# Kernel tuning notes

Measured on AMD Instinct MI355X. Metric: run time of the kernel, lower is better.

Reference implementation:

```python
import jax, jax.numpy as jnp
import numpy as np

C, CH, H = 128, 32, 4  # c_in, c_hidden, n_head


def _layer_norm(x, w, b, eps=1e-5):
    mu = jnp.mean(x, axis=-1, keepdims=True)
    var = jnp.var(x, axis=-1, keepdims=True)
    return (x - mu) * jax.lax.rsqrt(var + eps) * w + b


def _tri_attn(x, ln_w, ln_b, wq, wk, wv, wz, wg, bg, wo, bo):
    # x: [B, I, J, C]; attention runs over J independently for each row I
    B, I, J, _ = x.shape
    x = _layer_norm(x, ln_w, ln_b)
    q = (x @ wq).reshape(B, I, J, H, CH) * (CH ** -0.5)
    k = (x @ wk).reshape(B, I, J, H, CH)
    v = (x @ wv).reshape(B, I, J, H, CH)
    # learned pairwise triangle bias: [B, I, J, H] -> [B, 1, H, I, J]
    tb = jnp.transpose(x @ wz, (0, 3, 1, 2))[:, None]
    scores = jnp.einsum('biqhd,bikhd->bihqk', q, k) + tb  # [B, I, H, J, J]
    a = jax.nn.softmax(scores, axis=-1)
    o = jnp.einsum('bihqk,bikhd->biqhd', a, v)
    g = jax.nn.sigmoid(x @ wg + bg).reshape(B, I, J, H, CH)
    o = (o * g).reshape(B, I, J, H * CH)
    return o @ wo + bo


def setup_inputs() -> dict:
    key = jax.random.key(0)
    ks = jax.random.split(key, 16)
    B, N = 1, 256
    inp = {'cmap': jax.random.normal(ks[0], (B, C, N, N), jnp.float32)}
    for i, p in enumerate(['s', 'e']):
        kq, kk, kv, kz, kg, ko = jax.random.split(ks[1 + i], 6)
        sd = 0.02
        inp[p + '_ln_w'] = jnp.ones((C,), jnp.float32)
        inp[p + '_ln_b'] = jnp.zeros((C,), jnp.float32)
        inp[p + '_wq'] = jax.random.normal(kq, (C, H * CH), jnp.float32) * sd
        inp[p + '_wk'] = jax.random.normal(kk, (C, H * CH), jnp.float32) * sd
        inp[p + '_wv'] = jax.random.normal(kv, (C, H * CH), jnp.float32) * sd
        inp[p + '_wz'] = jax.random.normal(kz, (C, H), jnp.float32) * sd
        inp[p + '_wg'] = jax.random.normal(kg, (C, H * CH), jnp.float32) * sd
        inp[p + '_bg'] = jnp.ones((H * CH,), jnp.float32)  # gating bias init = 1
        inp[p + '_wo'] = jax.random.normal(ko, (H * CH, C), jnp.float32) * sd
        inp[p + '_bo'] = jnp.zeros((C,), jnp.float32)
    return inp


def reference(cmap,
              s_ln_w, s_ln_b, s_wq, s_wk, s_wv, s_wz, s_wg, s_bg, s_wo, s_bo,
              e_ln_w, e_ln_b, e_wq, e_wk, e_wv, e_wz, e_wg, e_bg, e_wo, e_bo):
    # cmap: [B, C, I, J] -> channels last [B, I, J, C]
    x = jnp.transpose(cmap, (0, 2, 3, 1))
    # triangle attention around starting node (dropout is identity in eval)
    x = x + _tri_attn(x, s_ln_w, s_ln_b, s_wq, s_wk, s_wv, s_wz, s_wg, s_bg, s_wo, s_bo)
    # triangle attention around ending node: transpose I<->J, attend, transpose back
    xt = jnp.swapaxes(x, 1, 2)
    x = x + jnp.swapaxes(
        _tri_attn(xt, e_ln_w, e_ln_b, e_wq, e_wk, e_wv, e_wz, e_wg, e_bg, e_wo, e_bo), 1, 2)
    return jnp.transpose(x, (0, 3, 1, 2))
```

## Files before the change

### kernel.cpp

```cpp
#include <hip/hip_runtime.h>
#include <hip/hip_bf16.h>

#define NNX 256
#define CCX 128
#define HHX 4
#define CHDX 32
#define NIJ (NNX*NNX)

typedef __hip_bfloat16 bf16;
typedef __hip_bfloat162 bf162;
typedef __attribute__((ext_vector_type(8))) short short8v;
typedef __attribute__((ext_vector_type(4))) float float4v;
typedef __attribute__((ext_vector_type(4))) unsigned int uint4v;

__device__ __forceinline__ float4v MFMA(short8v a, short8v b, float4v c){
  return __builtin_amdgcn_mfma_f32_16x16x32_bf16(a, b, c, 0, 0, 0);
}

__device__ __forceinline__ unsigned pk2(float a, float b){
  unsigned short ua = __bfloat16_as_ushort(__float2bfloat16(a));
  unsigned short ub = __bfloat16_as_ushort(__float2bfloat16(b));
  return (unsigned)ua | ((unsigned)ub << 16);
}
__device__ __forceinline__ float ubf(unsigned short u){
  return __bfloat162float(__ushort_as_bfloat16(u));
}

__global__ __launch_bounds__(256) void k_tout(const float* __restrict__ x, float* __restrict__ out){
  __shared__ float t[32][33];
  const int i = blockIdx.z, jt = blockIdx.x, ct = blockIdx.y;
  const int tx = threadIdx.x, ty = threadIdx.y;
  #pragma unroll
  for(int k=0;k<32;k+=8){
    t[ty+k][tx] = x[((size_t)i*NNX + jt*32+ty+k)*CCX + ct*32 + tx];
  }
  __syncthreads();
  #pragma unroll
  for(int k=0;k<32;k+=8){
    out[(size_t)(ct*32+ty+k)*NIJ + (size_t)i*NNX + jt*32 + tx] = t[tx][ty+k];
  }
}

__global__ __launch_bounds__(256) void k_lntin(const float* __restrict__ cmap,
    const float* __restrict__ w, const float* __restrict__ b,
    const float* __restrict__ wz, float* __restrict__ x,
    bf16* __restrict__ xln, float* __restrict__ tb2){
  __shared__ float t[32][130];
  const int jt = blockIdx.x, i = blockIdx.y;
  const int tx = threadIdx.x, ty = threadIdx.y;
  #pragma unroll
  for(int kk=0; kk<16; ++kk){
    const int c = kk*8 + ty;
    t[tx][c] = cmap[(size_t)c*NIJ + (size_t)i*NNX + jt*32 + tx];
  }
  __syncthreads();
  const int tid = ty*32 + tx;
  const int row = tid >> 3, cs = tid & 7;
  const int c0 = cs*16;
  float v[16];
  #pragma unroll
  for(int u=0;u<16;++u) v[u] = t[row][c0+u];
  float s=0.f, s2=0.f;
  #pragma unroll
  for(int u=0;u<16;++u){ s += v[u]; s2 += v[u]*v[u]; }
  #pragma unroll
  for(int off=4; off>0; off>>=1){ s += __shfl_xor(s,off); s2 += __shfl_xor(s2,off); }
  const float mu = s*0.0078125f;
  const float var = s2*0.0078125f - mu*mu;
  const float rs = rsqrtf(var+1e-5f);
  const int r = i*NNX + jt*32 + row;
  float a[16];
  #pragma unroll
  for(int u=0;u<16;++u) a[u] = (v[u]-mu)*rs*w[c0+u]+b[c0+u];
  float* xd = x + (size_t)r*CCX + c0;
  #pragma unroll
  for(int u4=0;u4<4;++u4){
    float4 f4; f4.x=v[u4*4]; f4.y=v[u4*4+1]; f4.z=v[u4*4+2]; f4.w=v[u4*4+3];
    *(float4*)(xd + u4*4) = f4;
  }
  bf16* xl = xln + (size_t)r*CCX + c0;
  #pragma unroll
  for(int u8=0;u8<4;++u8){
    uint2 pw; pw.x = pk2(a[u8*4], a[u8*4+1]); pw.y = pk2(a[u8*4+2], a[u8*4+3]);
    *(uint2*)(xl + u8*4) = pw;
  }
  float acc[4] = {0.f,0.f,0.f,0.f};
  #pragma unroll
  for(int u=0;u<16;++u){
    #pragma unroll
    for(int hh=0;hh<4;++hh) acc[hh] += a[u]*wz[(c0+u)*4+hh];
  }
  #pragma unroll
  for(int off=4; off>0; off>>=1){
    #pragma unroll
    for(int hh=0;hh<4;++hh) acc[hh] += __shfl_xor(acc[hh], off);
  }
  if(cs==0){
    #pragma unroll
    for(int hh=0;hh<4;++hh) tb2[(size_t)hh*NIJ + r] = acc[hh];
  }
}

template<int TRANS>
__global__ __launch_bounds__(256) void k_lntb(const float* __restrict__ x,
    const float* __restrict__ w, const float* __restrict__ b,
    const float* __restrict__ wz, bf16* __restrict__ xln, float* __restrict__ tb2){
  const int r = blockIdx.x*4 + threadIdx.y;
  const int ii = r>>8, jj = r&255;
  const float* src = x + (size_t)(TRANS ? (jj*NNX+ii) : r)*CCX;
  const int c = threadIdx.x*2;
  float2 v = *(const float2*)(src+c);
  float s = v.x+v.y, s2 = v.x*v.x+v.y*v.y;
  #pragma unroll
  for(int off=32; off>0; off>>=1){ s += __shfl_xor(s,off); s2 += __shfl_xor(s2,off); }
  float mu = s*0.0078125f;
  float var = s2*0.0078125f - mu*mu;
  float rs = rsqrtf(var+1e-5f);
  float a0 = (v.x-mu)*rs*w[c]+b[c];
  float a1 = (v.y-mu)*rs*w[c+1]+b[c+1];
  bf162 hp; hp.x = __float2bfloat16(a0); hp.y = __float2bfloat16(a1);
  *(bf162*)(xln + (size_t)r*CCX + c) = hp;
  float acc[4];
  #pragma unroll
  for(int hh=0;hh<4;++hh) acc[hh] = a0*wz[c*4+hh] + a1*wz[(c+1)*4+hh];
  #pragma unroll
  for(int off=32; off>0; off>>=1){
    #pragma unroll
    for(int hh=0;hh<4;++hh) acc[hh] += __shfl_xor(acc[hh], off);
  }
  if(threadIdx.x==0){
    #pragma unroll
    for(int hh=0;hh<4;++hh) tb2[(size_t)hh*NIJ + r] = acc[hh];
  }
}

__global__ __launch_bounds__(256) void k_cvtw(const float* __restrict__ wq,
    const float* __restrict__ wk, const float* __restrict__ wv,
    const float* __restrict__ wg, const float* __restrict__ wo, bf16* __restrict__ wT){
  int idx = blockIdx.x*256 + threadIdx.x;
  if(idx < 65536){
    int n = idx >> 7, k = idx & 127;
    const float* W = (n<128)?wq:(n<256)?wk:(n<384)?wv:wg;
    wT[idx] = __float2bfloat16(W[k*CCX + (n&127)]);
  } else {
    int idx2 = idx - 65536;
    int n = idx2 >> 7, k = idx2 & 127;
    wT[idx] = __float2bfloat16(wo[k*CCX + n]);
  }
}

template<int SUB>
__device__ __forceinline__ void attn_sub(const int mb,
    const int lq, const int g, const int l,
    uint2 pgl, uint2 pgh,
    const char* qsb, char* ksb, const char* vtb,
    const float* tbq_base, bf16* __restrict__ obh){
  const int q0 = mb + SUB*16;
  const int q  = q0 + lq;
  short8v qf = *(const short8v*)(qsb + (size_t)q*80 + g*16);
  const float* tbq = tbq_base + (size_t)q*NNX;
  float4v s[16];
  #pragma unroll
  for(int t=0;t<16;++t){
    short8v ak = *(const short8v*)(ksb + (size_t)(t*16 + lq)*80 + g*16);
    float4v bb = *(const float4v*)(tbq + t*16 + g*4);
    s[t] = MFMA(ak, qf, bb);
  }
  float m = -1e30f;
  #pragma unroll
  for(int t=0;t<16;++t)
    m = fmaxf(m, fmaxf(fmaxf(s[t][0], s[t][1]), fmaxf(s[t][2], s[t][3])));
  m = fmaxf(m, __shfl_xor(m,16));
  m = fmaxf(m, __shfl_xor(m,32));
  float lsum = 0.f;
  #pragma unroll
  for(int t=0;t<16;++t){
    #pragma unroll
    for(int r=0;r<4;++r){ float e = __expf(s[t][r]-m); s[t][r]=e; lsum+=e; }
  }
  lsum += __shfl_xor(lsum,16);
  lsum += __shfl_xor(lsum,32);
  const float linv = 1.0f/lsum;
  #pragma unroll
  for(int dt=0; dt<2; ++dt){
    float4v acc = (float4v)(0.f);
    #pragma unroll
    for(int c=0;c<8;++c){
      const int vrow = dt*16 + lq;
      short8v av = *(const short8v*)(vtb + (size_t)vrow*512 + ((16*g + 64*c) ^ ((vrow&7)<<4)));
      uint4 pb;
      pb.x = pk2(s[2*c][0],   s[2*c][1]);
      pb.y = pk2(s[2*c][2],   s[2*c][3]);
      pb.z = pk2(s[2*c+1][0], s[2*c+1][1]);
      pb.w = pk2(s[2*c+1][2], s[2*c+1][3]);
      short8v bp;
      bp[0]=(short)(pb.x&0xffff); bp[1]=(short)(pb.x>>16);
      bp[2]=(short)(pb.y&0xffff); bp[3]=(short)(pb.y>>16);
      bp[4]=(short)(pb.z&0xffff); bp[5]=(short)(pb.z>>16);
      bp[6]=(short)(pb.w&0xffff); bp[7]=(short)(pb.w>>16);
      acc = MFMA(av, bp, acc);
    }
    const uint2 pg = dt ? pgh : pgl;
    float g0 = ubf((unsigned short)(pg.x & 0xffff));
    float g1 = ubf((unsigned short)(pg.x >> 16));
    float g2 = ubf((unsigned short)(pg.y & 0xffff));
    float g3 = ubf((unsigned short)(pg.y >> 16));
    float o0 = acc[0]*linv / (1.f + __expf(-g0));
    float o1 = acc[1]*linv / (1.f + __expf(-g1));
    float o2 = acc[2]*linv / (1.f + __expf(-g2));
    float o3 = acc[3]*linv / (1.f + __expf(-g3));
    uint2 pw; pw.x = pk2(o0,o1); pw.y = pk2(o2,o3);
    *(uint2*)(ksb + (size_t)(mb + lq*4 + 2*dt + (g>>1))*80 + 64 + (g&1)*8) = pw;
  }
  {
    const int r2 = l >> 2, c2 = l & 3;
    uint4v ow = *(const uint4v*)(ksb + (size_t)(mb + r2*4 + c2)*80 + 64);
    __builtin_nontemporal_store(ow, (uint4v*)(obh + (size_t)(q0 + r2)*CHDX + c2*8));
  }
}

__global__ __launch_bounds__(256,2) void k_fattn(const bf16* __restrict__ xln,
    const bf16* __restrict__ wT, const float* __restrict__ bg,
    const float* __restrict__ tb2, bf16* __restrict__ op){
  __shared__ unsigned short Qs[256*40];
  __shared__ unsigned short Ks[256*40];
  __shared__ unsigned short Vt[32*256];
  const int id = blockIdx.x;
  const int h = id >> 8, i = id & 255;
  const int tid = threadIdx.x;
  const int w = tid >> 6, l = tid & 63;
  const int lq = l & 15, g = l >> 4;
  const int mb = w*64;

  char* qsb = (char*)Qs;
  char* ksb = (char*)Ks;
  char* vtb = (char*)Vt;

  short8v bx[4][4];
  #pragma unroll
  for(int ms=0; ms<4; ++ms){
    const size_t row = (size_t)i*NNX + mb + ms*16 + lq;
    #pragma unroll
    for(int kc=0; kc<4; ++kc)
      bx[ms][kc] = *(const short8v*)(xln + row*CCX + kc*32 + g*8);
  }
  uint2 pgl[4], pgh[4];

  #pragma unroll
  for(int half=0; half<2; ++half){
    const int n0 = h*32 + half*16;
    float4v acc[4];
    #pragma unroll
    for(int ms=0; ms<4; ++ms) acc[ms] = (float4v)(0.f);
    #pragma unroll
    for(int kc=0; kc<4; ++kc){
      short8v aw = *(const short8v*)(wT + (size_t)(n0 + lq)*CCX + kc*32 + g*8);
      #pragma unroll
      for(int ms=0; ms<4; ++ms) acc[ms] = MFMA(aw, bx[ms][kc], acc[ms]);
    }
    #pragma unroll
    for(int ms=0; ms<4; ++ms){
      const int row = mb + ms*16 + lq;
      uint2 pw; pw.x = pk2(acc[ms][0]*0.17677669529663687f, acc[ms][1]*0.17677669529663687f);
                pw.y = pk2(acc[ms][2]*0.17677669529663687f, acc[ms][3]*0.17677669529663687f);
      *(uint2*)(qsb + (size_t)row*80 + half*32 + g*8) = pw;
    }
  }
  #pragma unroll
  for(int half=0; half<2; ++half){
    const int n0 = 128 + h*32 + half*16;
    float4v acc[4];
    #pragma unroll
    for(int ms=0; ms<4; ++ms) acc[ms] = (float4v)(0.f);
    #pragma unroll
    for(int kc=0; kc<4; ++kc){
      short8v aw = *(const short8v*)(wT + (size_t)(n0 + lq)*CCX + kc*32 + g*8);
      #pragma unroll
      for(int ms=0; ms<4; ++ms) acc[ms] = MFMA(aw, bx[ms][kc], acc[ms]);
    }
    #pragma unroll
    for(int ms=0; ms<4; ++ms){
      const int row = mb + ms*16 + lq;
      uint2 pw; pw.x = pk2(acc[ms][0], acc[ms][1]);
                pw.y = pk2(acc[ms][2], acc[ms][3]);
      *(uint2*)(ksb + (size_t)row*80 + half*32 + g*8) = pw;
    }
  }
  #pragma unroll
  for(int half=0; half<2; ++half){
    const int n0 = 256 + h*32 + half*16;
    float4v acc[4];
    #pragma unroll
    for(int ms=0; ms<4; ++ms) acc[ms] = (float4v)(0.f);
    #pragma unroll
    for(int kc=0; kc<4; ++kc){
      short8v aw = *(const short8v*)(wT + (size_t)(n0 + lq)*CCX + kc*32 + g*8);
      #pragma unroll
      for(int ms=0; ms<4; ++ms) acc[ms] = MFMA(aw, bx[ms][kc], acc[ms]);
    }
    #pragma unroll
    for(int ms=0; ms<4; ++ms){
      const int k = mb + ms*16 + lq;
      const int j = k & 31;
      const int kap = (k & ~31) + 8*((j>>2)&3) + 4*((j>>4)&1) + (j&3);
      #pragma unroll
      for(int r=0; r<4; ++r){
        const int d = half*16 + 4*g + r;
        const int off = d*512 + ((2*kap) ^ ((d&7)<<4));
        *(unsigned short*)(vtb + off) = __bfloat16_as_ushort(__float2bfloat16(acc[ms][r]));
      }
    }
  }
  #pragma unroll
  for(int half=0; half<2; ++half){
    const int n0 = 384 + h*32 + half*16;
    float4v acc[4];
    #pragma unroll
    for(int ms=0; ms<4; ++ms) acc[ms] = (float4v)(0.f);
    #pragma unroll
    for(int kc=0; kc<4; ++kc){
      short8v aw = *(const short8v*)(wT + (size_t)(n0 + lq)*CCX + kc*32 + g*8);
      #pragma unroll
      for(int ms=0; ms<4; ++ms) acc[ms] = MFMA(aw, bx[ms][kc], acc[ms]);
    }
    const float4 bg4 = *(const float4*)(bg + h*32 + half*16 + 4*g);
    #pragma unroll
    for(int ms=0; ms<4; ++ms){
      uint2 pw; pw.x = pk2(acc[ms][0]+bg4.x, acc[ms][1]+bg4.y);
                pw.y = pk2(acc[ms][2]+bg4.z, acc[ms][3]+bg4.w);
      if(half==0) pgl[ms] = pw; else pgh[ms] = pw;
    }
  }
  __syncthreads();

  bf16* obh = op + ((size_t)h*NIJ + (size_t)i*NNX)*CHDX;
  const float* tbq_base = tb2 + (size_t)h*NIJ;
  attn_sub<0>(mb, lq, g, l, pgl[0], pgh[0], qsb, ksb, vtb, tbq_base, obh);
  attn_sub<1>(mb, lq, g, l, pgl[1], pgh[1], qsb, ksb, vtb, tbq_base, obh);
  attn_sub<2>(mb, lq, g, l, pgl[2], pgh[2], qsb, ksb, vtb, tbq_base, obh);
  attn_sub<3>(mb, lq, g, l, pgl[3], pgh[3], qsb, ksb, vtb, tbq_base, obh);
}

template<int TRANS>
__global__ __launch_bounds__(256) void k_oprojm(const bf16* __restrict__ ob,
    const bf16* __restrict__ woT, const float* __restrict__ bo, float* __restrict__ x){
  const int tid = threadIdx.x;
  const int w = tid >> 6, l = tid & 63;
  const int lq = l & 15, g = l >> 4;
  const int mbase = blockIdx.x*128 + w*32;
  short8v bx[2][4];
  #pragma unroll
  for(int ms=0; ms<2; ++ms){
    const size_t mrow = mbase + ms*16 + lq;
    #pragma unroll
    for(int kc=0; kc<4; ++kc)
      bx[ms][kc] = *(const short8v*)(ob + ((size_t)kc*NIJ + mrow)*CHDX + g*8);
  }
  #pragma unroll
  for(int nj=0; nj<8; ++nj){
    float4v acc0 = (float4v)(0.f), acc1 = (float4v)(0.f);
    #pragma unroll
    for(int kc=0; kc<4; ++kc){
      short8v aw = *(const short8v*)(woT + (size_t)(nj*16 + lq)*CCX + kc*32 + g*8);
      acc0 = MFMA(aw, bx[0][kc], acc0);
      acc1 = MFMA(aw, bx[1][kc], acc1);
    }
    const int col = nj*16 + 4*g;
    const float4 bo4 = *(const float4*)(bo + col);
    #pragma unroll
    for(int ms=0; ms<2; ++ms){
      const int r = mbase + ms*16 + lq;
      const int ii = r>>8, jj = r&255;
      float* dst = x + (size_t)(TRANS ? (jj*NNX+ii) : r)*CCX + col;
      float4 xv = *(float4*)dst;
      xv.x += ((ms==0)?acc0[0]:acc1[0]) + bo4.x;
      xv.y += ((ms==0)?acc0[1]:acc1[1]) + bo4.y;
      xv.z += ((ms==0)?acc0[2]:acc1[2]) + bo4.z;
      xv.w += ((ms==0)?acc0[3]:acc1[3]) + bo4.w;
      *(float4*)dst = xv;
    }
  }
}

extern "C" void kernel_launch(void* const* d_in, const int* in_sizes, int n_in,
                              void* d_out, int out_size, void* d_ws, size_t ws_size,
                              hipStream_t stream){
  const float* cmap = (const float*)d_in[0];
  char* ws = (char*)d_ws;
  float* x   = (float*)(ws);
  bf16* xln  = (bf16*)(ws + 33554432);
  bf16* ob   = (bf16*)(ws + 50331648);
  float* tb2 = (float*)(ws + 117440512);
  bf16* wT   = (bf16*)d_out;
  bf16* woT  = wT + 65536;
  float* outp = (float*)d_out;

  for(int p=0;p<2;++p){
    const int b = 1 + 10*p;
    const float* lnw = (const float*)d_in[b+0];
    const float* lnb = (const float*)d_in[b+1];
    const float* wq  = (const float*)d_in[b+2];
    const float* wk  = (const float*)d_in[b+3];
    const float* wv  = (const float*)d_in[b+4];
    const float* wz  = (const float*)d_in[b+5];
    const float* wg  = (const float*)d_in[b+6];
    const float* bg  = (const float*)d_in[b+7];
    const float* wo  = (const float*)d_in[b+8];
    const float* bo  = (const float*)d_in[b+9];

    k_cvtw<<<320, 256, 0, stream>>>(wq, wk, wv, wg, wo, wT);

    if(p==0) k_lntin<<<dim3(8,NNX), dim3(32,8), 0, stream>>>(cmap, lnw, lnb, wz, x, xln, tb2);
    else     k_lntb<1><<<NIJ/4, dim3(64,4), 0, stream>>>(x, lnw, lnb, wz, xln, tb2);

    k_fattn<<<1024, 256, 0, stream>>>(xln, wT, bg, tb2, ob);

    if(p==0) k_oprojm<0><<<NIJ/128, 256, 0, stream>>>(ob, woT, bo, x);
    else     k_oprojm<1><<<NIJ/128, 256, 0, stream>>>(ob, woT, bo, x);
  }

  k_tout<<<dim3(8,4,NNX), dim3(32,8), 0, stream>>>(x, outp);
}
```

Baseline: 238.2 us.

## Keep Q fragments in registers via lane shuffles, drop Q LDS buffer

The Q projection results are no longer written to a shared-memory tile and read back. They are redistributed across lanes with shuffles into the MFMA operand layout and passed straight into the attention subroutine. Removing the 20 KB Q buffer lowers LDS use per block, and the launch bound is raised to request three blocks per CU. The block index mapping is also changed so the four heads of the same row are adjacent, which improves L2 reuse of the xln row. The cost is more register pressure from holding four Q fragments, which may spill under the tighter register budget.

```diff
diff --git a/kernel.cpp b/kernel.cpp
--- a/kernel.cpp
+++ b/kernel.cpp
@@ -152,13 +152,11 @@
 template<int SUB>
 __device__ __forceinline__ void attn_sub(const int mb,
     const int lq, const int g, const int l,
-    uint2 pgl, uint2 pgh,
-    const char* qsb, char* ksb, const char* vtb,
+    short8v qf, uint2 pgl, uint2 pgh,
+    char* ksb, const char* vtb,
     const float* tbq_base, bf16* __restrict__ obh){
   const int q0 = mb + SUB*16;
-  const int q  = q0 + lq;
-  short8v qf = *(const short8v*)(qsb + (size_t)q*80 + g*16);
-  const float* tbq = tbq_base + (size_t)q*NNX;
+  const float* tbq = tbq_base + (size_t)(q0 + lq)*NNX;
   float4v s[16];
   #pragma unroll
   for(int t=0;t<16;++t){
@@ -219,20 +217,18 @@
   }
 }
 
-__global__ __launch_bounds__(256,2) void k_fattn(const bf16* __restrict__ xln,
+__global__ __launch_bounds__(256,3) void k_fattn(const bf16* __restrict__ xln,
     const bf16* __restrict__ wT, const float* __restrict__ bg,
     const float* __restrict__ tb2, bf16* __restrict__ op){
-  __shared__ unsigned short Qs[256*40];
   __shared__ unsigned short Ks[256*40];
   __shared__ unsigned short Vt[32*256];
   const int id = blockIdx.x;
-  const int h = id >> 8, i = id & 255;
+  const int i = id >> 2, h = id & 3;
   const int tid = threadIdx.x;
   const int w = tid >> 6, l = tid & 63;
   const int lq = l & 15, g = l >> 4;
   const int mb = w*64;
 
-  char* qsb = (char*)Qs;
   char* ksb = (char*)Ks;
   char* vtb = (char*)Vt;
 
@@ -244,26 +240,41 @@
     for(int kc=0; kc<4; ++kc)
       bx[ms][kc] = *(const short8v*)(xln + row*CCX + kc*32 + g*8);
   }
+  uint4v qfr[4];
   uint2 pgl[4], pgh[4];
 
-  #pragma unroll
-  for(int half=0; half<2; ++half){
-    const int n0 = h*32 + half*16;
-    float4v acc[4];
-    #pragma unroll
-    for(int ms=0; ms<4; ++ms) acc[ms] = (float4v)(0.f);
-    #pragma unroll
-    for(int kc=0; kc<4; ++kc){
-      short8v aw = *(const short8v*)(wT + (size_t)(n0 + lq)*CCX + kc*32 + g*8);
-      #pragma unroll
-      for(int ms=0; ms<4; ++ms) acc[ms] = MFMA(aw, bx[ms][kc], acc[ms]);
-    }
+  {
+    uint2 pqa0[4], pqa1[4];
+    #pragma unroll
+    for(int half=0; half<2; ++half){
+      const int n0 = h*32 + half*16;
+      float4v acc[4];
+      #pragma unroll
+      for(int ms=0; ms<4; ++ms) acc[ms] = (float4v)(0.f);
+      #pragma unroll
+      for(int kc=0; kc<4; ++kc){
+        short8v aw = *(const short8v*)(wT + (size_t)(n0 + lq)*CCX + kc*32 + g*8);
+        #pragma unroll
+        for(int ms=0; ms<4; ++ms) acc[ms] = MFMA(aw, bx[ms][kc], acc[ms]);
+      }
+      #pragma unroll
+      for(int ms=0; ms<4; ++ms){
+        uint2 pw;
+        pw.x = pk2(acc[ms][0]*0.17677669529663687f, acc[ms][1]*0.17677669529663687f);
+        pw.y = pk2(acc[ms][2]*0.17677669529663687f, acc[ms][3]*0.17677669529663687f);
+        if(half==0) pqa0[ms] = pw; else pqa1[ms] = pw;
+      }
+    }
+    const int srcA = lq + 32*(g&1);
+    const int hsel = g >> 1;
     #pragma unroll
     for(int ms=0; ms<4; ++ms){
-      const int row = mb + ms*16 + lq;
-      uint2 pw; pw.x = pk2(acc[ms][0]*0.17677669529663687f, acc[ms][1]*0.17677669529663687f);
-                pw.y = pk2(acc[ms][2]*0.17677669529663687f, acc[ms][3]*0.17677669529663687f);
-      *(uint2*)(qsb + (size_t)row*80 + half*32 + g*8) = pw;
+      unsigned sx = hsel ? pqa1[ms].x : pqa0[ms].x;
+      unsigned sy = hsel ? pqa1[ms].y : pqa0[ms].y;
+      qfr[ms].x = __shfl(sx, srcA);
+      qfr[ms].y = __shfl(sy, srcA);
+      qfr[ms].z = __shfl(sx, srcA+16);
+      qfr[ms].w = __shfl(sy, srcA+16);
     }
   }
   #pragma unroll
@@ -335,10 +346,10 @@
 
   bf16* obh = op + ((size_t)h*NIJ + (size_t)i*NNX)*CHDX;
   const float* tbq_base = tb2 + (size_t)h*NIJ;
-  attn_sub<0>(mb, lq, g, l, pgl[0], pgh[0], qsb, ksb, vtb, tbq_base, obh);
-  attn_sub<1>(mb, lq, g, l, pgl[1], pgh[1], qsb, ksb, vtb, tbq_base, obh);
-  attn_sub<2>(mb, lq, g, l, pgl[2], pgh[2], qsb, ksb, vtb, tbq_base, obh);
-  attn_sub<3>(mb, lq, g, l, pgl[3], pgh[3], qsb, ksb, vtb, tbq_base, obh);
+  attn_sub<0>(mb, lq, g, l, __builtin_bit_cast(short8v, qfr[0]), pgl[0], pgh[0], ksb, vtb, tbq_base, obh);
+  attn_sub<1>(mb, lq, g, l, __builtin_bit_cast(short8v, qfr[1]), pgl[1], pgh[1], ksb, vtb, tbq_base, obh);
+  attn_sub<2>(mb, lq, g, l, __builtin_bit_cast(short8v, qfr[2]), pgl[2], pgh[2], ksb, vtb, tbq_base, obh);
+  attn_sub<3>(mb, lq, g, l, __builtin_bit_cast(short8v, qfr[3]), pgl[3], pgh[3], ksb, vtb, tbq_base, obh);
 }
 
 template<int TRANS>
```

New measurement: 308.6 us. 1.3x slower.
